# Performance work log

Hardware: AMD Instinct MI355X
Metric: run time of the kernel (lower is better)

The kernel has to match this reference:

```python
import jax, jax.numpy as jnp
import numpy as np

SCALING = 2.0  # lora_alpha / r = 32 / 16


def setup_inputs() -> dict:
    key = jax.random.key(0)
    ks = jax.random.split(key, 5)
    N, D, E, R = 8192, 4096, 8, 16
    x = jax.random.normal(ks[0], (N, D), dtype=jnp.float32)
    base_W = jax.random.normal(ks[1], (D, D), dtype=jnp.float32) * (1.0 / np.sqrt(D))
    gate_W = jax.random.normal(ks[2], (E, D), dtype=jnp.float32) * (1.0 / np.sqrt(D))
    A = jax.random.normal(ks[3], (E, R, D), dtype=jnp.float32) * 0.01
    B = jax.random.normal(ks[4], (D, R), dtype=jnp.float32)[None] * jnp.ones((E, 1, 1)) * 0.01
    return {"x": x, "base_W": base_W, "gate_W": gate_W, "A": A, "B": B, "top_k": 2}


def reference(x, base_W, gate_W, A, B, top_k):
    N, D = x.shape
    E = gate_W.shape[0]
    # base linear (torch Linear: y = x @ W.T)
    result = x @ base_W.T
    # gate: top-k logits, softmax over the k selected (in fp32, cast back)
    gate_logits = x @ gate_W.T                      # [N, E]
    top_vals, top_idx = jax.lax.top_k(gate_logits, top_k)  # [N, k]
    w = jax.nn.softmax(top_vals.astype(jnp.float32), axis=-1).astype(x.dtype)
    # dense per-token per-expert routing weight (0 if not selected)
    w_full = jnp.zeros((N, E), dtype=x.dtype).at[
        jnp.arange(N)[:, None], top_idx].add(w)    # [N, E]
    # all-expert LoRA (matches the original dense loop over experts)
    ax = jnp.einsum('nd,erd->ner', x, A)            # [N, E, r]
    bx = jnp.einsum('ner,eor->neo', ax, B)          # [N, E, D]
    result = result + SCALING * jnp.einsum('neo,ne->no', bx, w_full)
    return result
```

## Files before the change

### kernel.cpp

```cpp
#include <hip/hip_runtime.h>
#include <math.h>


#define NTOK 8192
#define DIM  4096
#define NEXP 8
#define RANK 16
#define KAUG (NEXP * RANK)
#define KSPLIT 4
#define NKT  ((DIM + KAUG) / 64)

typedef __bf16 bf16x8 __attribute__((ext_vector_type(8)));
typedef float  f32x4  __attribute__((ext_vector_type(4)));

__device__ __forceinline__ unsigned short f2bf(float f) {
    union { float f; unsigned int u; } v;
    v.f = f;
    unsigned int u = v.u;
    return (unsigned short)((u + 0x7fffu + ((u >> 16) & 1u)) >> 16);
}

__global__ __launch_bounds__(256) void k_cvt(
    const float4* __restrict__ in, ushort4* __restrict__ outv, int n4)
{
    int i = blockIdx.x * 256 + threadIdx.x;
    if (i < n4) {
        float4 v = in[i];
        outv[i] = make_ushort4(f2bf(v.x), f2bf(v.y), f2bf(v.z), f2bf(v.w));
    }
}

__global__ __launch_bounds__(256) void k_bt(
    const float* __restrict__ B, unsigned short* __restrict__ Bt)
{
    int idx = blockIdx.x * 256 + threadIdx.x;
    int o = idx >> 7;
    int j = idx & 127;
    int e = j >> 4;
    int r = j & 15;
    Bt[idx] = f2bf(B[((size_t)e * DIM + o) * RANK + r]);
}

__global__ __launch_bounds__(256) void k_gate(
    const float* __restrict__ x,
    const float* __restrict__ gW,
    float4* __restrict__ gate_out,
    ushort4* __restrict__ xb4)
{
    __shared__ float xs[DIM];
    __shared__ float logits[NEXP];
    const int n = blockIdx.x;

    const float4* xr = (const float4*)(x + (size_t)n * DIM);
    ushort4* xw = xb4 + (size_t)n * (DIM / 4);
    for (int c = threadIdx.x; c < DIM / 4; c += 256) {
        float4 v = xr[c];
        xs[4 * c + 0] = v.x;
        xs[4 * c + 1] = v.y;
        xs[4 * c + 2] = v.z;
        xs[4 * c + 3] = v.w;
        xw[c] = make_ushort4(f2bf(v.x), f2bf(v.y), f2bf(v.z), f2bf(v.w));
    }
    __syncthreads();

    const int wave = threadIdx.x >> 6;
    const int lane = threadIdx.x & 63;
    for (int e = wave; e < NEXP; e += 4) {
        const float* g = gW + (size_t)e * DIM;
        float s = 0.f;
        for (int i = lane; i < DIM; i += 64) s += xs[i] * g[i];
        #pragma unroll
        for (int off = 32; off; off >>= 1) s += __shfl_down(s, off);
        if (lane == 0) logits[e] = s;
    }
    __syncthreads();

    if (threadIdx.x == 0) {
        int e0 = 0; float v0 = logits[0];
        #pragma unroll
        for (int e = 1; e < NEXP; ++e)
            if (logits[e] > v0) { v0 = logits[e]; e0 = e; }
        int e1 = -1; float v1 = -INFINITY;
        #pragma unroll
        for (int e = 0; e < NEXP; ++e)
            if (e != e0 && logits[e] > v1) { v1 = logits[e]; e1 = e; }
        float b = __expf(v1 - v0);
        float w0 = 1.f / (1.f + b);
        float w1 = 1.f - w0;
        gate_out[n] = make_float4((float)e0, (float)e1, w0, w1);
    }
}

__device__ __forceinline__ void stage_lds(
    const unsigned short* gbase, int strideElems,
    unsigned short* ldsBase, int wave, int lane)
{
    const int l8 = lane >> 3;
    const int c8 = ((lane & 7) ^ l8) << 3;
    #pragma unroll
    for (int q = 0; q < 4; ++q) {
        const int r = wave * 32 + q * 8;
        const unsigned short* gp = gbase + (size_t)(r + l8) * strideElems + c8;
        unsigned short* lp = ldsBase + r * 64;
        __builtin_amdgcn_global_load_lds(
            (const __attribute__((address_space(1))) void*)gp,
            (__attribute__((address_space(3))) void*)lp,
            16, 0, 0);
    }
}

__device__ __forceinline__ void mfma_step(
    const unsigned short* As, const unsigned short* Bs,
    int waveM, int waveN, int lane, f32x4 acc[4][4])
{
    const int quad = lane >> 4;
    const int l15  = lane & 15;
    const int x7   = l15 & 7;
    #pragma unroll
    for (int s = 0; s < 2; ++s) {
        const int chunk = (s << 2) | quad;
        const int po = ((chunk ^ x7) << 3);
        bf16x8 af[4], bfv[4];
        #pragma unroll
        for (int i = 0; i < 4; ++i)
            af[i] = *(const bf16x8*)(As + (waveM * 64 + i * 16 + l15) * 64 + po);
        #pragma unroll
        for (int j = 0; j < 4; ++j)
            bfv[j] = *(const bf16x8*)(Bs + (waveN * 64 + j * 16 + l15) * 64 + po);
        #pragma unroll
        for (int i = 0; i < 4; ++i)
            #pragma unroll
            for (int j = 0; j < 4; ++j)
                acc[i][j] = __builtin_amdgcn_mfma_f32_16x16x32_bf16(
                    af[i], bfv[j], acc[i][j], 0, 0, 0);
    }
}

__global__ __launch_bounds__(256) void k_ax(
    const unsigned short* __restrict__ xb,
    const unsigned short* __restrict__ Ab,
    float* __restrict__ axPart)
{
    __shared__ __align__(16) unsigned short As[128 * 64];
    __shared__ __align__(16) unsigned short Bs[128 * 64];
    const int tid  = threadIdx.x;
    const int wave = tid >> 6, lane = tid & 63;
    const int waveM = wave >> 1, waveN = wave & 1;
    const int rowBase = blockIdx.x * 128;
    const int ks = blockIdx.y;
    const int k0 = ks * (DIM / KSPLIT);

    f32x4 acc[4][4] = {};

    for (int it = 0; it < (DIM / KSPLIT) / 64; ++it) {
        stage_lds(xb + (size_t)rowBase * DIM + k0 + it * 64, DIM, As, wave, lane);
        stage_lds(Ab + (size_t)0 * DIM       + k0 + it * 64, DIM, Bs, wave, lane);
        __syncthreads();
        mfma_step(As, Bs, waveM, waveN, lane, acc);
        __syncthreads();
    }

    float* outp = axPart + (size_t)ks * NTOK * KAUG;
    const int quad = lane >> 4, l15 = lane & 15;
    #pragma unroll
    for (int i = 0; i < 4; ++i) {
        #pragma unroll
        for (int j = 0; j < 4; ++j) {
            const int gc = waveN * 64 + j * 16 + l15;
            #pragma unroll
            for (int t = 0; t < 4; ++t) {
                const int gr = rowBase + waveM * 64 + i * 16 + quad * 4 + t;
                outp[(size_t)gr * KAUG + gc] = acc[i][j][t];
            }
        }
    }
}

__global__ __launch_bounds__(256) void k_scale(
    const float* __restrict__ axPart,
    const float4* __restrict__ gate_out,
    unsigned short* __restrict__ cB)
{
    int idx = blockIdx.x * 256 + threadIdx.x;
    int n = idx >> 7;
    int j = idx & 127;
    float s = 0.f;
    #pragma unroll
    for (int ks = 0; ks < KSPLIT; ++ks)
        s += axPart[(size_t)ks * NTOK * KAUG + idx];
    float4 g = gate_out[n];
    int e  = j >> 4;
    int e0 = (int)g.x;
    int e1 = (int)g.y;
    float scale = (e == e0) ? 2.f * g.z : (e == e1) ? 2.f * g.w : 0.f;
    cB[idx] = f2bf(scale * s);
}

__global__ __launch_bounds__(512) void k_main(
    const unsigned short* __restrict__ xb,
    const unsigned short* __restrict__ Wb,
    const unsigned short* __restrict__ cB,
    const unsigned short* __restrict__ Bt,
    float* __restrict__ out)
{
    __shared__ __align__(16) unsigned short sA[2][256 * 64];
    __shared__ __align__(16) unsigned short sB[2][256 * 64];

    const int tid  = threadIdx.x;
    const int wave = tid >> 6, lane = tid & 63;
    const int wm = wave >> 2, wn = wave & 3;
    const int quad = lane >> 4, l15 = lane & 15;
    const int x7 = l15 & 7;

    const int bid = blockIdx.x;
    const int swz = (bid & 7) * 64 + (bid >> 3);
    const int rowBase = (swz >> 4) * 256;
    const int colBase = (swz & 15) * 256;

    const unsigned short* aMain = xb + (size_t)rowBase * DIM;
    const unsigned short* bMain = Wb + (size_t)colBase * DIM;
    const unsigned short* aLora = cB + (size_t)rowBase * KAUG;
    const unsigned short* bLora = Bt + (size_t)colBase * KAUG;

    const int l8 = lane >> 3;
    const int c8 = ((lane & 7) ^ l8) << 3;

    auto stageT = [&](int t, int half, bool isA) {
        if (t >= NKT) return;
        unsigned short* ldsR = isA ? &sA[t & 1][0] : &sB[t & 1][0];
        const unsigned short* g;
        int stride;
        if (t < DIM / 64) { g = (isA ? aMain : bMain) + t * 64;              stride = DIM;  }
        else              { g = (isA ? aLora : bLora) + (t - DIM / 64) * 64; stride = KAUG; }
        #pragma unroll
        for (int qq = 0; qq < 2; ++qq) {
            const int r0 = half * 128 + qq * 64 + wave * 8;
            const unsigned short* gp = g + (size_t)(r0 + l8) * stride + c8;
            unsigned short* lp = ldsR + r0 * 64;
            __builtin_amdgcn_global_load_lds(
                (const __attribute__((address_space(1))) void*)gp,
                (__attribute__((address_space(3))) void*)lp,
                16, 0, 0);
        }
    };

    f32x4 acc[8][4] = {};

    stageT(0, 0, true);  stageT(0, 1, true);
    stageT(0, 0, false); stageT(0, 1, false);
    stageT(1, 0, false); stageT(1, 1, false);
    asm volatile("s_waitcnt vmcnt(4)" ::: "memory");
    __builtin_amdgcn_s_barrier();

    #pragma unroll 2
    for (int k = 0; k < NKT; ++k) {
        const unsigned short* At = &sA[k & 1][0];
        const unsigned short* Bl = &sB[k & 1][0];
        bf16x8 bFr[4][2];
        #pragma unroll
        for (int q = 0; q < 4; ++q) {
            bf16x8 aFr[2][2];
            #pragma unroll
            for (int mi = 0; mi < 2; ++mi)
                #pragma unroll
                for (int ksl = 0; ksl < 2; ++ksl) {
                    const int r  = wm * 128 + (q * 2 + mi) * 16 + l15;
                    const int ch = ksl * 4 + quad;
                    aFr[mi][ksl] = *(const bf16x8*)(At + r * 64 + ((ch ^ x7) << 3));
                }
            if (q == 0) {
                #pragma unroll
                for (int nf = 0; nf < 4; ++nf)
                    #pragma unroll
                    for (int ksl = 0; ksl < 2; ++ksl) {
                        const int r  = wn * 64 + nf * 16 + l15;
                        const int ch = ksl * 4 + quad;
                        bFr[nf][ksl] = *(const bf16x8*)(Bl + r * 64 + ((ch ^ x7) << 3));
                    }
            }
            if      (q == 0) stageT(k + 1, 0, true);
            else if (q == 1) stageT(k + 1, 1, true);
            else if (q == 2) stageT(k + 2, 0, false);
            else             stageT(k + 2, 1, false);

            __builtin_amdgcn_s_barrier();
            asm volatile("s_waitcnt lgkmcnt(0)" ::: "memory");
            __builtin_amdgcn_sched_barrier(0);
            __builtin_amdgcn_s_setprio(1);
            #pragma unroll
            for (int mi = 0; mi < 2; ++mi)
                #pragma unroll
                for (int nf = 0; nf < 4; ++nf)
                    #pragma unroll
                    for (int ksl = 0; ksl < 2; ++ksl)
                        acc[q * 2 + mi][nf] = __builtin_amdgcn_mfma_f32_16x16x32_bf16(
                            aFr[mi][ksl], bFr[nf][ksl], acc[q * 2 + mi][nf], 0, 0, 0);
            __builtin_amdgcn_s_setprio(0);
            __builtin_amdgcn_sched_barrier(0);
            if (q == 3) {
                if (k == NKT - 2)
                    asm volatile("s_waitcnt vmcnt(0)" ::: "memory");
                else if (k < NKT - 2)
                    asm volatile("s_waitcnt vmcnt(4)" ::: "memory");
            }
            __builtin_amdgcn_s_barrier();
        }
    }

    #pragma unroll
    for (int mf = 0; mf < 8; ++mf) {
        #pragma unroll
        for (int nf = 0; nf < 4; ++nf) {
            const int gc = colBase + wn * 64 + nf * 16 + l15;
            #pragma unroll
            for (int t = 0; t < 4; ++t) {
                const int gr = rowBase + wm * 128 + mf * 16 + quad * 4 + t;
                out[(size_t)gr * DIM + gc] = acc[mf][nf][t];
            }
        }
    }
}

extern "C" void kernel_launch(void* const* d_in, const int* in_sizes, int n_in,
                              void* d_out, int out_size, void* d_ws, size_t ws_size,
                              hipStream_t stream) {
    (void)in_sizes; (void)n_in; (void)out_size; (void)ws_size;

    const float* x  = (const float*)d_in[0];
    const float* bW = (const float*)d_in[1];
    const float* gW = (const float*)d_in[2];
    const float* A  = (const float*)d_in[3];
    const float* B  = (const float*)d_in[4];
    float* out = (float*)d_out;

    char* ws = (char*)d_ws;
    float4*         gate_out = (float4*)ws;
    unsigned short* xb = (unsigned short*)(ws + (1u << 17));
    unsigned short* Wb = xb + (size_t)NTOK * DIM;
    unsigned short* Ab = Wb + (size_t)DIM * DIM;
    unsigned short* Bt = Ab + (size_t)KAUG * DIM;
    unsigned short* cB = Bt + (size_t)DIM * KAUG;
    float*      axPart = (float*)(cB + (size_t)NTOK * KAUG);

    k_gate<<<NTOK, 256, 0, stream>>>(x, gW, gate_out, (ushort4*)xb);
    k_cvt <<<(DIM * DIM / 4 + 255) / 256, 256, 0, stream>>>(
        (const float4*)bW, (ushort4*)Wb, DIM * DIM / 4);
    k_cvt <<<(KAUG * DIM / 4 + 255) / 256, 256, 0, stream>>>(
        (const float4*)A, (ushort4*)Ab, KAUG * DIM / 4);
    k_bt  <<<(DIM * KAUG) / 256, 256, 0, stream>>>(B, Bt);
    k_ax  <<<dim3(NTOK / 128, KSPLIT), 256, 0, stream>>>(xb, Ab, axPart);
    k_scale<<<(NTOK * KAUG) / 256, 256, 0, stream>>>(axPart, gate_out, cB);
    k_main<<<dim3(512), dim3(512), 0, stream>>>(xb, Wb, cB, Bt, out);
}
```

Before: 691.6 us.

## Rework gate kernel to four tokens per wave and vectorize helper kernels

The gate kernel now has each wave handle four tokens. It reads x and the gate weights as float4 straight from global memory, with no LDS staging, and reduces with xor shuffles, so the launch count drops 16x and each gate-weight load is reused across four tokens. The B transpose and the scale kernels now use float4/ushort4 vector loads and stores. The main GEMM block-to-tile mapping changes so that each XCD owns a group of row tiles, which should improve L2 reuse of x. An extra lgkmcnt wait is added in the pipeline. These are several unrelated tweaks, and the gate kernel's higher register use could lower its occupancy.

```diff
diff --git a/kernel.cpp b/kernel.cpp
--- a/kernel.cpp
+++ b/kernel.cpp
@@ -31,14 +31,16 @@
 }
 
 __global__ __launch_bounds__(256) void k_bt(
-    const float* __restrict__ B, unsigned short* __restrict__ Bt)
-{
-    int idx = blockIdx.x * 256 + threadIdx.x;
+    const float* __restrict__ B, ushort4* __restrict__ Bt4)
+{
+    int i4 = blockIdx.x * 256 + threadIdx.x;
+    int idx = i4 * 4;
     int o = idx >> 7;
     int j = idx & 127;
     int e = j >> 4;
     int r = j & 15;
-    Bt[idx] = f2bf(B[((size_t)e * DIM + o) * RANK + r]);
+    const float4 v = *(const float4*)(B + ((size_t)e * DIM + o) * RANK + r);
+    Bt4[i4] = make_ushort4(f2bf(v.x), f2bf(v.y), f2bf(v.z), f2bf(v.w));
 }
 
 __global__ __launch_bounds__(256) void k_gate(
@@ -47,47 +49,70 @@
     float4* __restrict__ gate_out,
     ushort4* __restrict__ xb4)
 {
-    __shared__ float xs[DIM];
-    __shared__ float logits[NEXP];
-    const int n = blockIdx.x;
-
-    const float4* xr = (const float4*)(x + (size_t)n * DIM);
-    ushort4* xw = xb4 + (size_t)n * (DIM / 4);
-    for (int c = threadIdx.x; c < DIM / 4; c += 256) {
-        float4 v = xr[c];
-        xs[4 * c + 0] = v.x;
-        xs[4 * c + 1] = v.y;
-        xs[4 * c + 2] = v.z;
-        xs[4 * c + 3] = v.w;
-        xw[c] = make_ushort4(f2bf(v.x), f2bf(v.y), f2bf(v.z), f2bf(v.w));
-    }
-    __syncthreads();
-
     const int wave = threadIdx.x >> 6;
     const int lane = threadIdx.x & 63;
-    for (int e = wave; e < NEXP; e += 4) {
-        const float* g = gW + (size_t)e * DIM;
-        float s = 0.f;
-        for (int i = lane; i < DIM; i += 64) s += xs[i] * g[i];
-        #pragma unroll
-        for (int off = 32; off; off >>= 1) s += __shfl_down(s, off);
-        if (lane == 0) logits[e] = s;
-    }
-    __syncthreads();
-
-    if (threadIdx.x == 0) {
-        int e0 = 0; float v0 = logits[0];
-        #pragma unroll
-        for (int e = 1; e < NEXP; ++e)
-            if (logits[e] > v0) { v0 = logits[e]; e0 = e; }
-        int e1 = -1; float v1 = -INFINITY;
-        #pragma unroll
-        for (int e = 0; e < NEXP; ++e)
-            if (e != e0 && logits[e] > v1) { v1 = logits[e]; e1 = e; }
-        float b = __expf(v1 - v0);
-        float w0 = 1.f / (1.f + b);
-        float w1 = 1.f - w0;
-        gate_out[n] = make_float4((float)e0, (float)e1, w0, w1);
+    const int n0 = blockIdx.x * 16 + wave * 4;
+
+    const float4* __restrict__ g4 = (const float4*)gW;
+    const float4* xr0 = (const float4*)(x + (size_t)(n0 + 0) * DIM);
+    const float4* xr1 = (const float4*)(x + (size_t)(n0 + 1) * DIM);
+    const float4* xr2 = (const float4*)(x + (size_t)(n0 + 2) * DIM);
+    const float4* xr3 = (const float4*)(x + (size_t)(n0 + 3) * DIM);
+    ushort4* xw0 = xb4 + (size_t)(n0 + 0) * (DIM / 4);
+    ushort4* xw1 = xb4 + (size_t)(n0 + 1) * (DIM / 4);
+    ushort4* xw2 = xb4 + (size_t)(n0 + 2) * (DIM / 4);
+    ushort4* xw3 = xb4 + (size_t)(n0 + 3) * (DIM / 4);
+
+    float s[4][8];
+    #pragma unroll
+    for (int t = 0; t < 4; ++t)
+        #pragma unroll
+        for (int e = 0; e < 8; ++e) s[t][e] = 0.f;
+
+    for (int j = 0; j < 16; ++j) {
+        const int idx = j * 64 + lane;
+        float4 v0 = xr0[idx];
+        float4 v1 = xr1[idx];
+        float4 v2 = xr2[idx];
+        float4 v3 = xr3[idx];
+        #pragma unroll
+        for (int e = 0; e < 8; ++e) {
+            const float4 g = g4[e * (DIM / 4) + idx];
+            s[0][e] += v0.x * g.x + v0.y * g.y + v0.z * g.z + v0.w * g.w;
+            s[1][e] += v1.x * g.x + v1.y * g.y + v1.z * g.z + v1.w * g.w;
+            s[2][e] += v2.x * g.x + v2.y * g.y + v2.z * g.z + v2.w * g.w;
+            s[3][e] += v3.x * g.x + v3.y * g.y + v3.z * g.z + v3.w * g.w;
+        }
+        xw0[idx] = make_ushort4(f2bf(v0.x), f2bf(v0.y), f2bf(v0.z), f2bf(v0.w));
+        xw1[idx] = make_ushort4(f2bf(v1.x), f2bf(v1.y), f2bf(v1.z), f2bf(v1.w));
+        xw2[idx] = make_ushort4(f2bf(v2.x), f2bf(v2.y), f2bf(v2.z), f2bf(v2.w));
+        xw3[idx] = make_ushort4(f2bf(v3.x), f2bf(v3.y), f2bf(v3.z), f2bf(v3.w));
+    }
+
+    #pragma unroll
+    for (int t = 0; t < 4; ++t)
+        #pragma unroll
+        for (int e = 0; e < 8; ++e)
+            #pragma unroll
+            for (int off = 32; off; off >>= 1)
+                s[t][e] += __shfl_xor(s[t][e], off);
+
+    #pragma unroll
+    for (int t = 0; t < 4; ++t) {
+        if (lane == t) {
+            int e0 = 0; float v0 = s[t][0];
+            #pragma unroll
+            for (int e = 1; e < 8; ++e)
+                if (s[t][e] > v0) { v0 = s[t][e]; e0 = e; }
+            int e1 = -1; float v1 = -INFINITY;
+            #pragma unroll
+            for (int e = 0; e < 8; ++e)
+                if (e != e0 && s[t][e] > v1) { v1 = s[t][e]; e1 = e; }
+            float b = __expf(v1 - v0);
+            float w0 = 1.f / (1.f + b);
+            float w1 = 1.f - w0;
+            gate_out[n0 + t] = make_float4((float)e0, (float)e1, w0, w1);
+        }
     }
 }
 
@@ -179,21 +204,25 @@
 __global__ __launch_bounds__(256) void k_scale(
     const float* __restrict__ axPart,
     const float4* __restrict__ gate_out,
-    unsigned short* __restrict__ cB)
-{
-    int idx = blockIdx.x * 256 + threadIdx.x;
+    ushort4* __restrict__ cB4)
+{
+    int i4 = blockIdx.x * 256 + threadIdx.x;
+    int idx = i4 * 4;
     int n = idx >> 7;
     int j = idx & 127;
-    float s = 0.f;
-    #pragma unroll
-    for (int ks = 0; ks < KSPLIT; ++ks)
-        s += axPart[(size_t)ks * NTOK * KAUG + idx];
+    float4 s = make_float4(0.f, 0.f, 0.f, 0.f);
+    #pragma unroll
+    for (int ks = 0; ks < KSPLIT; ++ks) {
+        const float4 v = *(const float4*)(axPart + (size_t)ks * NTOK * KAUG + idx);
+        s.x += v.x; s.y += v.y; s.z += v.z; s.w += v.w;
+    }
     float4 g = gate_out[n];
     int e  = j >> 4;
     int e0 = (int)g.x;
     int e1 = (int)g.y;
     float scale = (e == e0) ? 2.f * g.z : (e == e1) ? 2.f * g.w : 0.f;
-    cB[idx] = f2bf(scale * s);
+    cB4[i4] = make_ushort4(f2bf(scale * s.x), f2bf(scale * s.y),
+                           f2bf(scale * s.z), f2bf(scale * s.w));
 }
 
 __global__ __launch_bounds__(512) void k_main(
@@ -212,10 +241,10 @@
     const int quad = lane >> 4, l15 = lane & 15;
     const int x7 = l15 & 7;
 
-    const int bid = blockIdx.x;
-    const int swz = (bid & 7) * 64 + (bid >> 3);
-    const int rowBase = (swz >> 4) * 256;
-    const int colBase = (swz & 15) * 256;
+    const int bid  = blockIdx.x;
+    const int xcd  = bid & 7, slot = bid >> 3;
+    const int rowBase = (xcd * 4 + (slot & 3)) * 256;
+    const int colBase = (slot >> 2) * 256;
 
     const unsigned short* aMain = xb + (size_t)rowBase * DIM;
     const unsigned short* bMain = Wb + (size_t)colBase * DIM;
@@ -283,6 +312,9 @@
             else if (q == 2) stageT(k + 2, 0, false);
             else             stageT(k + 2, 1, false);
 
+            if (q == 0)
+                asm volatile("s_waitcnt lgkmcnt(8)" ::: "memory");
+
             __builtin_amdgcn_s_barrier();
             asm volatile("s_waitcnt lgkmcnt(0)" ::: "memory");
             __builtin_amdgcn_sched_barrier(0);
@@ -342,13 +374,14 @@
     unsigned short* cB = Bt + (size_t)DIM * KAUG;
     float*      axPart = (float*)(cB + (size_t)NTOK * KAUG);
 
-    k_gate<<<NTOK, 256, 0, stream>>>(x, gW, gate_out, (ushort4*)xb);
+    k_gate<<<NTOK / 16, 256, 0, stream>>>(x, gW, gate_out, (ushort4*)xb);
     k_cvt <<<(DIM * DIM / 4 + 255) / 256, 256, 0, stream>>>(
         (const float4*)bW, (ushort4*)Wb, DIM * DIM / 4);
     k_cvt <<<(KAUG * DIM / 4 + 255) / 256, 256, 0, stream>>>(
         (const float4*)A, (ushort4*)Ab, KAUG * DIM / 4);
-    k_bt  <<<(DIM * KAUG) / 256, 256, 0, stream>>>(B, Bt);
+    k_bt  <<<(DIM * KAUG / 4) / 256, 256, 0, stream>>>(B, (ushort4*)Bt);
     k_ax  <<<dim3(NTOK / 128, KSPLIT), 256, 0, stream>>>(xb, Ab, axPart);
-    k_scale<<<(NTOK * KAUG) / 256, 256, 0, stream>>>(axPart, gate_out, cB);
+    k_scale<<<(NTOK * KAUG / 4) / 256, 256, 0, stream>>>(
+        axPart, gate_out, (ushort4*)cB);
     k_main<<<dim3(512), dim3(512), 0, stream>>>(xb, Wb, cB, Bt, out);
 }
```

Measured after the change: 583.4 us. 15.7% less time.
